# Kernel optimization log

Measured on AMD Instinct MI355X. Metric: run time of the kernel, lower is better.

Reference implementation:

```python
import jax, jax.numpy as jnp
import numpy as np

N, IN_DIM, E_DIM, H, D = 10000, 128, 32, 4, 32
NE = 640000
OUT_DIM = D  # out Linear maps H*D -> out_dim == D here (32)


def setup_inputs() -> dict:
    key = jax.random.key(0)
    ks = jax.random.split(key, 12)
    HD = H * D
    s = lambda k, sh, fan: jax.random.normal(k, sh, jnp.float32) / np.sqrt(fan)
    return {
        "x": jax.random.normal(ks[0], (N, IN_DIM), jnp.float32),
        "edge_index": jax.random.randint(ks[1], (2, NE), 0, N),
        "edge_attr": jax.random.normal(ks[2], (NE, E_DIM), jnp.float32),
        "Wq": s(ks[3], (IN_DIM, HD), IN_DIM), "bq": jnp.zeros((HD,), jnp.float32),
        "Wk": s(ks[4], (IN_DIM, HD), IN_DIM), "bk": jnp.zeros((HD,), jnp.float32),
        "Wv": s(ks[5], (IN_DIM, HD), IN_DIM), "bv": jnp.zeros((HD,), jnp.float32),
        "We": s(ks[6], (E_DIM, HD), E_DIM), "be": jnp.zeros((HD,), jnp.float32),
        "Wo": s(ks[7], (HD, OUT_DIM), HD), "bo": jnp.zeros((OUT_DIM,), jnp.float32),
    }


def reference(x, edge_index, edge_attr, Wq, bq, Wk, bk, Wv, bv, We, be, Wo, bo):
    n = x.shape[0]
    Q = (x @ Wq + bq).reshape(-1, H, D)
    K = (x @ Wk + bk).reshape(-1, H, D)
    V = (x @ Wv + bv).reshape(-1, H, D)
    Ef = (edge_attr @ We + be).reshape(-1, H, D)
    src, dst = edge_index[0], edge_index[1]
    # per-edge scores [E, H]: QK dot over src/dst gather + E self dot
    scores = (jnp.einsum('ehd,ehd->eh', Q[src], K[dst])
              + jnp.einsum('ehd,ehd->eh', Ef, Ef)) / np.sqrt(D).astype(np.float32)
    alpha = jax.nn.softmax(scores, axis=-1)  # softmax over heads (as in source)
    out_e = (alpha[..., None] * V[dst]).reshape(-1, H * D)  # [E, H*D]
    out_e = out_e @ Wo + bo  # [E, out_dim]
    # scatter-mean by source node
    sums = jax.ops.segment_sum(out_e, src, num_segments=n)
    cnt = jax.ops.segment_sum(jnp.ones((out_e.shape[0],), out_e.dtype), src, num_segments=n)
    return sums / jnp.maximum(cnt, 1.0)[:, None]
```

## Files before the change

kernel.cpp:

```cpp
#include <hip/hip_runtime.h>

#define NN      10000
#define IN_DIM  128
#define E_DIM   32
#define NH      4
#define DH      32
#define HD      128
#define NE_     640000
#define OUT_DIM 32
#define SCAN_T  1024
#define CHUNK   10
#define NTILES  (NN / 16)
#define NTASKS  (NTILES * 3)
#define QKVP_BLKS  469
#define HIST_BLKS  (NE_ / 256)
#define EE_BLKS    (NE_ / 256)

typedef __attribute__((ext_vector_type(8))) short bf16x8;
typedef __attribute__((ext_vector_type(4))) float f32x4;

static __device__ __forceinline__ unsigned short f32_to_bf16_rne(float f) {
    unsigned u = __float_as_uint(f);
    return (unsigned short)((u + 0x7fffu + ((u >> 16) & 1u)) >> 16);
}
static __device__ __forceinline__ float bf16_bits_to_f32(unsigned short h) {
    return __uint_as_float(((unsigned)h) << 16);
}

__global__ __launch_bounds__(256) void prep_kernel(
    const float* __restrict__ Wq, const float* __restrict__ Wk,
    const float* __restrict__ Wv, const float* __restrict__ Wo,
    const float* __restrict__ bv, const float* __restrict__ We,
    const int*   __restrict__ ei,
    unsigned short* __restrict__ wfh, unsigned short* __restrict__ wfl,
    unsigned short* __restrict__ wefh, unsigned short* __restrict__ wefl,
    float* __restrict__ bp,
    int* __restrict__ deg, int* __restrict__ rank)
{
    const int blk = blockIdx.x;
    const int t = threadIdx.x;

    if (blk < 24) {
        const int tid = blk * 256 + t;
        const int l = tid & 63;
        const int ts = tid >> 6;
        const int s = ts & 3, tt = ts >> 2;
        const int col = (tt & 7) * 16 + (l & 15);
        if (tt < 16) {
            const float* __restrict__ W = (tt < 8) ? Wq : Wk;
            #pragma unroll
            for (int j = 0; j < 8; ++j) {
                const int k = s * 32 + (l >> 4) * 8 + j;
                const float w = W[k * HD + col];
                const unsigned short hi = f32_to_bf16_rne(w);
                wfh[tid * 8 + j] = hi;
                wfl[tid * 8 + j] = f32_to_bf16_rne(w - bf16_bits_to_f32(hi));
            }
        } else {
            const int h = col & 3, oo = col >> 2;
            #pragma unroll
            for (int j = 0; j < 8; ++j) {
                const int k = s * 32 + (l >> 4) * 8 + j;
                float acc = 0.f;
                #pragma unroll
                for (int d2 = 0; d2 < DH; ++d2)
                    acc = fmaf(Wv[k * HD + h * DH + d2],
                               Wo[(h * DH + d2) * OUT_DIM + oo], acc);
                const unsigned short hi = f32_to_bf16_rne(acc);
                wfh[tid * 8 + j] = hi;
                wfl[tid * 8 + j] = f32_to_bf16_rne(acc - bf16_bits_to_f32(hi));
            }
        }
    } else if (blk < 26) {
        const int tid = (blk - 24) * 256 + t;
        const int l = tid & 63, tt = tid >> 6;
        #pragma unroll
        for (int j = 0; j < 8; ++j) {
            const int k = (l >> 4) * 8 + j;
            const int d = tt * 16 + (l & 15);
            const float w = We[k * HD + d];
            const unsigned short hi = f32_to_bf16_rne(w);
            wefh[tid * 8 + j] = hi;
            wefl[tid * 8 + j] = f32_to_bf16_rne(w - bf16_bits_to_f32(hi));
        }
    } else if (blk == 26) {
        if (t < HD) {
            const int h = t & 3, oo = t >> 2;
            float b = 0.f;
            #pragma unroll
            for (int d2 = 0; d2 < DH; ++d2)
                b = fmaf(bv[h * DH + d2], Wo[(h * DH + d2) * OUT_DIM + oo], b);
            bp[t] = b;
        }
    } else {
        const int e = (blk - 27) * 256 + t;
        rank[e] = atomicAdd(&deg[ei[e]], 1);
    }
}

__global__ __launch_bounds__(SCAN_T) void scan_kernel(
    const int* __restrict__ deg, int* __restrict__ off)
{
    __shared__ int wsum[16];
    const int t = threadIdx.x;
    const int lane = t & 63, w = t >> 6;
    const int base = t * CHUNK;
    int v[CHUNK];
    int sum = 0;
    #pragma unroll
    for (int i = 0; i < CHUNK; ++i) {
        const int idx = base + i;
        v[i] = (idx < NN) ? deg[idx] : 0;
        sum += v[i];
    }
    int incl = sum;
    #pragma unroll
    for (int dlt = 1; dlt < 64; dlt <<= 1) {
        const int nb = __shfl_up(incl, dlt, 64);
        if (lane >= dlt) incl += nb;
    }
    if (lane == 63) wsum[w] = incl;
    __syncthreads();
    if (w == 0) {
        const int val = (lane < 16) ? wsum[lane] : 0;
        int wi = val;
        #pragma unroll
        for (int dlt = 1; dlt < 16; dlt <<= 1) {
            const int nb = __shfl_up(wi, dlt, 64);
            if (lane >= dlt) wi += nb;
        }
        if (lane < 16) wsum[lane] = wi - val;
    }
    __syncthreads();
    int run = wsum[w] + (incl - sum);
    #pragma unroll
    for (int i = 0; i < CHUNK; ++i) {
        const int idx = base + i;
        if (idx < NN) { off[idx] = run; run += v[i]; }
    }
}

__global__ __launch_bounds__(256) void mm_kernel(
    const float* __restrict__ x,
    const unsigned short* __restrict__ wfh, const unsigned short* __restrict__ wfl,
    const float* __restrict__ bq, const float* __restrict__ bk,
    const float* __restrict__ bp,
    float* __restrict__ Q, unsigned short* __restrict__ KPTb,
    const float* __restrict__ ea,
    const unsigned short* __restrict__ wefh, const unsigned short* __restrict__ wefl,
    const float* __restrict__ be,
    const int* __restrict__ ei,
    const int* __restrict__ off, const int* __restrict__ rank,
    float4* __restrict__ pay)
{
    const int lane = threadIdx.x & 63;
    const int wave = threadIdx.x >> 6;

    if (blockIdx.x < QKVP_BLKS) {
        const int task = blockIdx.x * 4 + wave;
        if (task >= NTASKS) return;
        const int nt = task / 3, cg = task - nt * 3;
        const int node = nt * 16 + (lane & 15);
        const int kc = lane >> 4;

        bf16x8 xh0, xl0, xh1, xl1, xh2, xl2, xh3, xl3;
#define SPL(VH, VL, I, VAL) { \
    const unsigned short hh = f32_to_bf16_rne(VAL); \
    VH[I] = (short)hh; VL[I] = (short)f32_to_bf16_rne((VAL) - bf16_bits_to_f32(hh)); }
#define LOAD_X(S, VH, VL) { \
    const float* xr = x + (size_t)node * IN_DIM + (S) * 32 + kc * 8; \
    const float4 a0 = *reinterpret_cast<const float4*>(xr); \
    const float4 a1 = *reinterpret_cast<const float4*>(xr + 4); \
    SPL(VH, VL, 0, a0.x) SPL(VH, VL, 1, a0.y) SPL(VH, VL, 2, a0.z) SPL(VH, VL, 3, a0.w) \
    SPL(VH, VL, 4, a1.x) SPL(VH, VL, 5, a1.y) SPL(VH, VL, 6, a1.z) SPL(VH, VL, 7, a1.w) }
        LOAD_X(0, xh0, xl0) LOAD_X(1, xh1, xl1) LOAD_X(2, xh2, xl2) LOAD_X(3, xh3, xl3)
#undef LOAD_X
#undef SPL

        const float* __restrict__ bb = (cg == 0) ? bq : (cg == 1) ? bk : bp;

#define KSTEP(S, FB, FB2, XH, XL) { \
    const bf16x8 wh = *reinterpret_cast<const bf16x8*>((FB)  + (S) * 64 * 8); \
    const bf16x8 wl = *reinterpret_cast<const bf16x8*>((FB2) + (S) * 64 * 8); \
    acc = __builtin_amdgcn_mfma_f32_16x16x32_bf16(wh, XH, acc, 0, 0, 0); \
    acc = __builtin_amdgcn_mfma_f32_16x16x32_bf16(wh, XL, acc, 0, 0, 0); \
    acc = __builtin_amdgcn_mfma_f32_16x16x32_bf16(wl, XH, acc, 0, 0, 0); }

#define TILE(TLOC) { \
    const unsigned short* fb  = wfh + ((((cg * 8 + TLOC) * 4) * 64 + lane) << 3); \
    const unsigned short* fb2 = wfl + ((((cg * 8 + TLOC) * 4) * 64 + lane) << 3); \
    f32x4 acc = {0.f, 0.f, 0.f, 0.f}; \
    KSTEP(0, fb, fb2, xh0, xl0) KSTEP(1, fb, fb2, xh1, xl1) \
    KSTEP(2, fb, fb2, xh2, xl2) KSTEP(3, fb, fb2, xh3, xl3) \
    const float4 b4 = *reinterpret_cast<const float4*>(bb + (TLOC) * 16 + (kc << 2)); \
    const float o0 = acc[0] + b4.x, o1 = acc[1] + b4.y; \
    const float o2 = acc[2] + b4.z, o3 = acc[3] + b4.w; \
    const int j0 = (TLOC) * 16 + (kc << 2); \
    if (cg == 0) { \
        *reinterpret_cast<float4*>(Q + (size_t)node * HD + j0) = \
            make_float4(o0, o1, o2, o3); \
    } else { \
        unsigned short* dp = KPTb + (size_t)node * 256 + j0 * 2 + ((cg == 1) ? 0 : 4); \
        *reinterpret_cast<ushort4*>(dp) = make_ushort4( \
            f32_to_bf16_rne(o0), f32_to_bf16_rne(o1), \
            f32_to_bf16_rne(o2), f32_to_bf16_rne(o3)); \
    } }

        TILE(0) TILE(1) TILE(2) TILE(3) TILE(4) TILE(5) TILE(6) TILE(7)
#undef TILE
#undef KSTEP
        return;
    }

    const int base = (blockIdx.x - QKVP_BLKS) * 256 + wave * 64;

    const int src  = ei[base + lane];
    const int dstn = ei[NE_ + base + lane];
    const int pos  = off[src] + rank[base + lane];

    const int erow = lane & 15;
    const int kc = lane >> 4;
    bf16x8 ah0, ah1, ah2, ah3;
#define LOAD_A(AT, VAR) { \
    const float* ar = ea + (size_t)(base + AT * 16 + erow) * E_DIM + kc * 8; \
    const float4 a0 = *reinterpret_cast<const float4*>(ar); \
    const float4 a1 = *reinterpret_cast<const float4*>(ar + 4); \
    VAR[0] = (short)f32_to_bf16_rne(a0.x); VAR[1] = (short)f32_to_bf16_rne(a0.y); \
    VAR[2] = (short)f32_to_bf16_rne(a0.z); VAR[3] = (short)f32_to_bf16_rne(a0.w); \
    VAR[4] = (short)f32_to_bf16_rne(a1.x); VAR[5] = (short)f32_to_bf16_rne(a1.y); \
    VAR[6] = (short)f32_to_bf16_rne(a1.z); VAR[7] = (short)f32_to_bf16_rne(a1.w); }
    LOAD_A(0, ah0) LOAD_A(1, ah1) LOAD_A(2, ah2) LOAD_A(3, ah3)
#undef LOAD_A

    float p00 = 0.f, p01 = 0.f, p02 = 0.f, p03 = 0.f;
    float p10 = 0.f, p11 = 0.f, p12 = 0.f, p13 = 0.f;
    float p20 = 0.f, p21 = 0.f, p22 = 0.f, p23 = 0.f;
    float p30 = 0.f, p31 = 0.f, p32 = 0.f, p33 = 0.f;

#define AT_BODY(AT, H, WHI, WLO, BE4) { \
    f32x4 acc = {0.f, 0.f, 0.f, 0.f}; \
    acc = __builtin_amdgcn_mfma_f32_16x16x32_bf16(WLO, ah##AT, acc, 0, 0, 0); \
    acc = __builtin_amdgcn_mfma_f32_16x16x32_bf16(WHI, ah##AT, acc, 0, 0, 0); \
    const float e0 = acc[0] + BE4.x, e1 = acc[1] + BE4.y; \
    const float e2 = acc[2] + BE4.z, e3 = acc[3] + BE4.w; \
    p##AT##H += e0 * e0 + e1 * e1 + e2 * e2 + e3 * e3; }

#define TILE(T, H) { \
    const bf16x8 whi = *reinterpret_cast<const bf16x8*>(wefh + ((T * 64 + lane) << 3)); \
    const bf16x8 wlo = *reinterpret_cast<const bf16x8*>(wefl + ((T * 64 + lane) << 3)); \
    const float4 be4 = *reinterpret_cast<const float4*>(be + T * 16 + ((lane >> 4) << 2)); \
    AT_BODY(0, H, whi, wlo, be4) AT_BODY(1, H, whi, wlo, be4) \
    AT_BODY(2, H, whi, wlo, be4) AT_BODY(3, H, whi, wlo, be4) }

    TILE(0, 0) TILE(1, 0) TILE(2, 1) TILE(3, 1)
    TILE(4, 2) TILE(5, 2) TILE(6, 3) TILE(7, 3)
#undef TILE
#undef AT_BODY

#define RED(AT, H) \
    float r##AT##H = p##AT##H; \
    r##AT##H += __shfl_xor(r##AT##H, 16, 64); \
    r##AT##H += __shfl_xor(r##AT##H, 32, 64);
    RED(0, 0) RED(0, 1) RED(0, 2) RED(0, 3)
    RED(1, 0) RED(1, 1) RED(1, 2) RED(1, 3)
    RED(2, 0) RED(2, 1) RED(2, 2) RED(2, 3)
    RED(3, 0) RED(3, 1) RED(3, 2) RED(3, 3)
#undef RED

    const int at4 = lane >> 4;
#define SEL(H) ((at4 & 2) ? ((at4 & 1) ? r3##H : r2##H) : ((at4 & 1) ? r1##H : r0##H))
    const float w0 = SEL(0), w1 = SEL(1), w2 = SEL(2), w3 = SEL(3);
#undef SEL

    pay[pos] = make_float4(__int_as_float(dstn), w0 - w3, w1 - w3, w2 - w3);
}

static __device__ __forceinline__ float edge_term(
    const uint4 u, const float4 pc, const float4 q4, const int h)
{
    const float scale = 0.17677669529663687f;
    const float k0 = __uint_as_float(u.x << 16);
    const float k1 = __uint_as_float(u.x & 0xffff0000u);
    const float k2 = __uint_as_float(u.y << 16);
    const float k3 = __uint_as_float(u.y & 0xffff0000u);
    float p =           q4.x * k0;
    p = fmaf(q4.y, k1, p); p = fmaf(q4.z, k2, p); p = fmaf(q4.w, k3, p);
    p += __shfl_xor(p, 1, 64);
    p += __shfl_xor(p, 2, 64);
    p += __shfl_xor(p, 4, 64);
    const float b  = __shfl_xor(p, 8, 64);
    const float e0 = (h & 1) ? b : p;
    const float e1 = (h & 1) ? p : b;
    const float o0 = __shfl_xor(e0, 16, 64);
    const float o1 = __shfl_xor(e1, 16, 64);
    const float qk0 = (h & 2) ? o0 : e0;
    const float qk1 = (h & 2) ? o1 : e1;
    const float qk2 = (h & 2) ? e0 : o0;
    const float qk3 = (h & 2) ? e1 : o1;

    const float s0 = (qk0 + pc.y) * scale;
    const float s1 = (qk1 + pc.z) * scale;
    const float s2 = (qk2 + pc.w) * scale;
    const float s3 = qk3 * scale;
    const float mx = fmaxf(fmaxf(s0, s1), fmaxf(s2, s3));
    const float a0 = __expf(s0 - mx), a1 = __expf(s1 - mx);
    const float a2 = __expf(s2 - mx), a3 = __expf(s3 - mx);
    const float inv = 1.f / (a0 + a1 + a2 + a3);
    const float p0 = __uint_as_float(u.z << 16);
    const float p1 = __uint_as_float(u.z & 0xffff0000u);
    const float p2 = __uint_as_float(u.w << 16);
    const float p3 = __uint_as_float(u.w & 0xffff0000u);
    return fmaf(a0, p0, fmaf(a1, p1, fmaf(a2, p2, a3 * p3))) * inv;
}

__global__ __launch_bounds__(256) void fused_gather_kernel(
    const int* __restrict__ off, const int* __restrict__ deg,
    const float4* __restrict__ pay,
    const float* __restrict__ Q, const unsigned short* __restrict__ KPTb,
    const float* __restrict__ bo, float* __restrict__ out)
{
    __shared__ float red[8][OUT_DIM];
    const int n = blockIdx.x;
    const int d = deg[n];
    const int start = off[n];
    const int tid = threadIdx.x;
    const int g = tid >> 5, o = tid & 31;
    const int h = o >> 3;

    const float4 q4 = *reinterpret_cast<const float4*>(Q + (size_t)n * HD + o * 4);

    float acc = 0.f;
    float4 pc0 = make_float4(0.f, 0.f, 0.f, 0.f);
    float4 pc1 = make_float4(0.f, 0.f, 0.f, 0.f);
    if (g < d)     pc0 = pay[start + g];
    if (g + 8 < d) pc1 = pay[start + g + 8];

    for (int i = g; i < d; i += 16) {
        float4 pn0 = make_float4(0.f, 0.f, 0.f, 0.f);
        float4 pn1 = make_float4(0.f, 0.f, 0.f, 0.f);
        if (i + 16 < d) pn0 = pay[start + i + 16];
        if (i + 24 < d) pn1 = pay[start + i + 24];

        const int dst0 = __float_as_int(pc0.x);
        const int dst1 = __float_as_int(pc1.x);
        const uint4 u0 = *reinterpret_cast<const uint4*>(KPTb + (size_t)dst0 * 256 + o * 8);
        const uint4 u1 = *reinterpret_cast<const uint4*>(KPTb + (size_t)dst1 * 256 + o * 8);

        acc += edge_term(u0, pc0, q4, h);
        if (i + 8 < d)
            acc += edge_term(u1, pc1, q4, h);

        pc0 = pn0; pc1 = pn1;
    }
    red[g][o] = acc;
    __syncthreads();
    if (tid < 32) {
        const float s = red[0][o] + red[1][o] + red[2][o] + red[3][o]
                      + red[4][o] + red[5][o] + red[6][o] + red[7][o];
        out[(size_t)n * OUT_DIM + o] = (d > 0) ? (s / (float)d + bo[o]) : 0.f;
    }
}

extern "C" void kernel_launch(void* const* d_in, const int* in_sizes, int n_in,
                              void* d_out, int out_size, void* d_ws, size_t ws_size,
                              hipStream_t stream)
{
    const float* x   = (const float*)d_in[0];
    const int*   ei  = (const int*)  d_in[1];
    const float* ea  = (const float*)d_in[2];
    const float* Wq  = (const float*)d_in[3];
    const float* bq  = (const float*)d_in[4];
    const float* Wk  = (const float*)d_in[5];
    const float* bk  = (const float*)d_in[6];
    const float* Wv  = (const float*)d_in[7];
    const float* bv  = (const float*)d_in[8];
    const float* We  = (const float*)d_in[9];
    const float* be  = (const float*)d_in[10];
    const float* Wo  = (const float*)d_in[11];
    const float* bo  = (const float*)d_in[12];
    float* out = (float*)d_out;

    float*  Q    = (float*)d_ws;
    float4* pay  = (float4*)(Q + (size_t)NN * HD);
    unsigned short* KPTb = (unsigned short*)(pay + NE_);
    float*  bp   = (float*)(KPTb + (size_t)NN * 256);
    unsigned short* wefh = (unsigned short*)(bp + HD);
    unsigned short* wefl = wefh + 8 * 64 * 8;
    unsigned short* wfh  = wefl + 8 * 64 * 8;
    unsigned short* wfl  = wfh + 24 * 4 * 64 * 8;
    int* rank = (int*)(wfl + 24 * 4 * 64 * 8);
    int* deg  = rank + NE_;
    int* off  = deg + NN;

    hipMemsetAsync(deg, 0, NN * sizeof(int), stream);

    prep_kernel<<<27 + HIST_BLKS, 256, 0, stream>>>(Wq, Wk, Wv, Wo, bv, We, ei,
                                                    wfh, wfl, wefh, wefl, bp,
                                                    deg, rank);
    scan_kernel<<<1, SCAN_T, 0, stream>>>(deg, off);
    mm_kernel<<<QKVP_BLKS + EE_BLKS, 256, 0, stream>>>(x, wfh, wfl, bq, bk, bp,
                                                       Q, KPTb, ea, wefh, wefl,
                                                       be, ei, off, rank, pay);
    fused_gather_kernel<<<NN, 256, 0, stream>>>(off, deg, pay, Q, KPTb, bo, out);
}
```

Baseline: 134.0 us.

## Write edge payloads coalesced with sorted id indirection; widen gather to 16 lanes per edge

The edge kernel now writes each edge's payload (dst and score terms) coalesced, in original edge order, and scatters only a 4-byte edge id into the per-source sorted slot. The gather kernel reads the id, then the payload, which adds a level of indirection. In exchange the 16-byte scattered writes become 4-byte ones. The gather now uses 16 threads per edge, each handling 8 features and two output columns, so 16 edges are in flight per block. Biases are folded into the MFMA accumulator initialisation, and the self-dot is rewritten as an FMA chain.

Measured after the change: 127.9 us. 4.5% less time.

```diff
diff --git a/kernel.cpp b/kernel.cpp
--- a/kernel.cpp
+++ b/kernel.cpp
@@ -26,6 +26,8 @@
 static __device__ __forceinline__ float bf16_bits_to_f32(unsigned short h) {
     return __uint_as_float(((unsigned)h) << 16);
 }
+static __device__ __forceinline__ float blo(unsigned u) { return __uint_as_float(u << 16); }
+static __device__ __forceinline__ float bhi(unsigned u) { return __uint_as_float(u & 0xffff0000u); }
 
 __global__ __launch_bounds__(256) void prep_kernel(
     const float* __restrict__ Wq, const float* __restrict__ Wk,
@@ -151,7 +153,7 @@
     const float* __restrict__ be,
     const int* __restrict__ ei,
     const int* __restrict__ off, const int* __restrict__ rank,
-    float4* __restrict__ pay)
+    float4* __restrict__ eev, int* __restrict__ ids)
 {
     const int lane = threadIdx.x & 63;
     const int wave = threadIdx.x >> 6;
@@ -189,21 +191,19 @@
 #define TILE(TLOC) { \
     const unsigned short* fb  = wfh + ((((cg * 8 + TLOC) * 4) * 64 + lane) << 3); \
     const unsigned short* fb2 = wfl + ((((cg * 8 + TLOC) * 4) * 64 + lane) << 3); \
-    f32x4 acc = {0.f, 0.f, 0.f, 0.f}; \
+    const float4 b4 = *reinterpret_cast<const float4*>(bb + (TLOC) * 16 + (kc << 2)); \
+    f32x4 acc = {b4.x, b4.y, b4.z, b4.w}; \
     KSTEP(0, fb, fb2, xh0, xl0) KSTEP(1, fb, fb2, xh1, xl1) \
     KSTEP(2, fb, fb2, xh2, xl2) KSTEP(3, fb, fb2, xh3, xl3) \
-    const float4 b4 = *reinterpret_cast<const float4*>(bb + (TLOC) * 16 + (kc << 2)); \
-    const float o0 = acc[0] + b4.x, o1 = acc[1] + b4.y; \
-    const float o2 = acc[2] + b4.z, o3 = acc[3] + b4.w; \
     const int j0 = (TLOC) * 16 + (kc << 2); \
     if (cg == 0) { \
         *reinterpret_cast<float4*>(Q + (size_t)node * HD + j0) = \
-            make_float4(o0, o1, o2, o3); \
+            make_float4(acc[0], acc[1], acc[2], acc[3]); \
     } else { \
         unsigned short* dp = KPTb + (size_t)node * 256 + j0 * 2 + ((cg == 1) ? 0 : 4); \
         *reinterpret_cast<ushort4*>(dp) = make_ushort4( \
-            f32_to_bf16_rne(o0), f32_to_bf16_rne(o1), \
-            f32_to_bf16_rne(o2), f32_to_bf16_rne(o3)); \
+            f32_to_bf16_rne(acc[0]), f32_to_bf16_rne(acc[1]), \
+            f32_to_bf16_rne(acc[2]), f32_to_bf16_rne(acc[3])); \
     } }
 
         TILE(0) TILE(1) TILE(2) TILE(3) TILE(4) TILE(5) TILE(6) TILE(7)
@@ -238,12 +238,11 @@
     float p30 = 0.f, p31 = 0.f, p32 = 0.f, p33 = 0.f;
 
 #define AT_BODY(AT, H, WHI, WLO, BE4) { \
-    f32x4 acc = {0.f, 0.f, 0.f, 0.f}; \
+    f32x4 acc = {BE4.x, BE4.y, BE4.z, BE4.w}; \
     acc = __builtin_amdgcn_mfma_f32_16x16x32_bf16(WLO, ah##AT, acc, 0, 0, 0); \
     acc = __builtin_amdgcn_mfma_f32_16x16x32_bf16(WHI, ah##AT, acc, 0, 0, 0); \
-    const float e0 = acc[0] + BE4.x, e1 = acc[1] + BE4.y; \
-    const float e2 = acc[2] + BE4.z, e3 = acc[3] + BE4.w; \
-    p##AT##H += e0 * e0 + e1 * e1 + e2 * e2 + e3 * e3; }
+    p##AT##H = fmaf(acc[0], acc[0], fmaf(acc[1], acc[1], \
+               fmaf(acc[2], acc[2], fmaf(acc[3], acc[3], p##AT##H)))); }
 
 #define TILE(T, H) { \
     const bf16x8 whi = *reinterpret_cast<const bf16x8*>(wefh + ((T * 64 + lane) << 3)); \
@@ -272,92 +271,98 @@
     const float w0 = SEL(0), w1 = SEL(1), w2 = SEL(2), w3 = SEL(3);
 #undef SEL
 
-    pay[pos] = make_float4(__int_as_float(dstn), w0 - w3, w1 - w3, w2 - w3);
-}
-
-static __device__ __forceinline__ float edge_term(
-    const uint4 u, const float4 pc, const float4 q4, const int h)
-{
-    const float scale = 0.17677669529663687f;
-    const float k0 = __uint_as_float(u.x << 16);
-    const float k1 = __uint_as_float(u.x & 0xffff0000u);
-    const float k2 = __uint_as_float(u.y << 16);
-    const float k3 = __uint_as_float(u.y & 0xffff0000u);
-    float p =           q4.x * k0;
-    p = fmaf(q4.y, k1, p); p = fmaf(q4.z, k2, p); p = fmaf(q4.w, k3, p);
-    p += __shfl_xor(p, 1, 64);
-    p += __shfl_xor(p, 2, 64);
-    p += __shfl_xor(p, 4, 64);
-    const float b  = __shfl_xor(p, 8, 64);
-    const float e0 = (h & 1) ? b : p;
-    const float e1 = (h & 1) ? p : b;
-    const float o0 = __shfl_xor(e0, 16, 64);
-    const float o1 = __shfl_xor(e1, 16, 64);
-    const float qk0 = (h & 2) ? o0 : e0;
-    const float qk1 = (h & 2) ? o1 : e1;
-    const float qk2 = (h & 2) ? e0 : o0;
-    const float qk3 = (h & 2) ? e1 : o1;
-
-    const float s0 = (qk0 + pc.y) * scale;
-    const float s1 = (qk1 + pc.z) * scale;
-    const float s2 = (qk2 + pc.w) * scale;
-    const float s3 = qk3 * scale;
-    const float mx = fmaxf(fmaxf(s0, s1), fmaxf(s2, s3));
-    const float a0 = __expf(s0 - mx), a1 = __expf(s1 - mx);
-    const float a2 = __expf(s2 - mx), a3 = __expf(s3 - mx);
-    const float inv = 1.f / (a0 + a1 + a2 + a3);
-    const float p0 = __uint_as_float(u.z << 16);
-    const float p1 = __uint_as_float(u.z & 0xffff0000u);
-    const float p2 = __uint_as_float(u.w << 16);
-    const float p3 = __uint_as_float(u.w & 0xffff0000u);
-    return fmaf(a0, p0, fmaf(a1, p1, fmaf(a2, p2, a3 * p3))) * inv;
+    eev[base + lane] = make_float4(__int_as_float(dstn), w0 - w3, w1 - w3, w2 - w3);
+    ids[pos] = base + lane;
 }
 
 __global__ __launch_bounds__(256) void fused_gather_kernel(
     const int* __restrict__ off, const int* __restrict__ deg,
-    const float4* __restrict__ pay,
+    const int* __restrict__ ids, const float4* __restrict__ eev,
     const float* __restrict__ Q, const unsigned short* __restrict__ KPTb,
     const float* __restrict__ bo, float* __restrict__ out)
 {
-    __shared__ float red[8][OUT_DIM];
+    __shared__ float red[16][OUT_DIM];
     const int n = blockIdx.x;
     const int d = deg[n];
     const int start = off[n];
     const int tid = threadIdx.x;
-    const int g = tid >> 5, o = tid & 31;
-    const int h = o >> 3;
-
-    const float4 q4 = *reinterpret_cast<const float4*>(Q + (size_t)n * HD + o * 4);
-
-    float acc = 0.f;
-    float4 pc0 = make_float4(0.f, 0.f, 0.f, 0.f);
-    float4 pc1 = make_float4(0.f, 0.f, 0.f, 0.f);
-    if (g < d)     pc0 = pay[start + g];
-    if (g + 8 < d) pc1 = pay[start + g + 8];
+    const int g = tid >> 4;
+    const int o16 = tid & 15;
+    const int h = o16 >> 2;
+    const float scale = 0.17677669529663687f;
+
+    const float* __restrict__ qrow = Q + (size_t)n * HD + o16 * 8;
+    const float4 qa = *reinterpret_cast<const float4*>(qrow);
+    const float4 qb = *reinterpret_cast<const float4*>(qrow + 4);
+
+    float acc0 = 0.f, acc1 = 0.f;
+
+    float4 pc = make_float4(0.f, 0.f, 0.f, 0.f);
+    int idn = 0;
+    if (g < d)      pc  = eev[ids[start + g]];
+    if (g + 16 < d) idn = ids[start + g + 16];
 
     for (int i = g; i < d; i += 16) {
-        float4 pn0 = make_float4(0.f, 0.f, 0.f, 0.f);
-        float4 pn1 = make_float4(0.f, 0.f, 0.f, 0.f);
-        if (i + 16 < d) pn0 = pay[start + i + 16];
-        if (i + 24 < d) pn1 = pay[start + i + 24];
-
-        const int dst0 = __float_as_int(pc0.x);
-        const int dst1 = __float_as_int(pc1.x);
-        const uint4 u0 = *reinterpret_cast<const uint4*>(KPTb + (size_t)dst0 * 256 + o * 8);
-        const uint4 u1 = *reinterpret_cast<const uint4*>(KPTb + (size_t)dst1 * 256 + o * 8);
-
-        acc += edge_term(u0, pc0, q4, h);
-        if (i + 8 < d)
-            acc += edge_term(u1, pc1, q4, h);
-
-        pc0 = pn0; pc1 = pn1;
-    }
-    red[g][o] = acc;
+        int idn2 = 0;
+        if (i + 32 < d) idn2 = ids[start + i + 32];
+        float4 pn = make_float4(0.f, 0.f, 0.f, 0.f);
+        if (i + 16 < d) pn = eev[idn];
+
+        const int dst = __float_as_int(pc.x);
+        const unsigned short* __restrict__ kp = KPTb + (size_t)dst * 256 + o16 * 16;
+        const uint4 u0 = *reinterpret_cast<const uint4*>(kp);
+        const uint4 u1 = *reinterpret_cast<const uint4*>(kp + 8);
+
+        float p =           qa.x * blo(u0.x);
+        p = fmaf(qa.y, bhi(u0.x), p);
+        p = fmaf(qa.z, blo(u0.y), p);
+        p = fmaf(qa.w, bhi(u0.y), p);
+        p = fmaf(qb.x, blo(u1.x), p);
+        p = fmaf(qb.y, bhi(u1.x), p);
+        p = fmaf(qb.z, blo(u1.y), p);
+        p = fmaf(qb.w, bhi(u1.y), p);
+        p += __shfl_xor(p, 1, 64);
+        p += __shfl_xor(p, 2, 64);
+        const float b  = __shfl_xor(p, 4, 64);
+        const float e0 = (h & 1) ? b : p;
+        const float e1 = (h & 1) ? p : b;
+        const float o0 = __shfl_xor(e0, 8, 64);
+        const float o1 = __shfl_xor(e1, 8, 64);
+        const float qk0 = (h & 2) ? o0 : e0;
+        const float qk1 = (h & 2) ? o1 : e1;
+        const float qk2 = (h & 2) ? e0 : o0;
+        const float qk3 = (h & 2) ? e1 : o1;
+
+        const float s0 = (qk0 + pc.y) * scale;
+        const float s1 = (qk1 + pc.z) * scale;
+        const float s2 = (qk2 + pc.w) * scale;
+        const float s3 = qk3 * scale;
+        const float mx = fmaxf(fmaxf(s0, s1), fmaxf(s2, s3));
+        const float a0 = __expf(s0 - mx), a1 = __expf(s1 - mx);
+        const float a2 = __expf(s2 - mx), a3 = __expf(s3 - mx);
+        const float inv = 1.f / (a0 + a1 + a2 + a3);
+
+        float c0 =          a0 * blo(u0.z);
+        c0 = fmaf(a1, bhi(u0.z), c0);
+        c0 = fmaf(a2, blo(u0.w), c0);
+        c0 = fmaf(a3, bhi(u0.w), c0);
+        float c1 =          a0 * blo(u1.z);
+        c1 = fmaf(a1, bhi(u1.z), c1);
+        c1 = fmaf(a2, blo(u1.w), c1);
+        c1 = fmaf(a3, bhi(u1.w), c1);
+        acc0 = fmaf(c0, inv, acc0);
+        acc1 = fmaf(c1, inv, acc1);
+
+        pc = pn; idn = idn2;
+    }
+    red[g][o16 * 2]     = acc0;
+    red[g][o16 * 2 + 1] = acc1;
     __syncthreads();
     if (tid < 32) {
-        const float s = red[0][o] + red[1][o] + red[2][o] + red[3][o]
-                      + red[4][o] + red[5][o] + red[6][o] + red[7][o];
-        out[(size_t)n * OUT_DIM + o] = (d > 0) ? (s / (float)d + bo[o]) : 0.f;
+        float s = 0.f;
+        #pragma unroll
+        for (int gg = 0; gg < 16; ++gg) s += red[gg][tid];
+        out[(size_t)n * OUT_DIM + tid] = (d > 0) ? (s / (float)d + bo[tid]) : 0.f;
     }
 }
 
@@ -381,15 +386,16 @@
     float* out = (float*)d_out;
 
     float*  Q    = (float*)d_ws;
-    float4* pay  = (float4*)(Q + (size_t)NN * HD);
-    unsigned short* KPTb = (unsigned short*)(pay + NE_);
+    float4* eev  = (float4*)(Q + (size_t)NN * HD);
+    unsigned short* KPTb = (unsigned short*)(eev + NE_);
     float*  bp   = (float*)(KPTb + (size_t)NN * 256);
     unsigned short* wefh = (unsigned short*)(bp + HD);
     unsigned short* wefl = wefh + 8 * 64 * 8;
     unsigned short* wfh  = wefl + 8 * 64 * 8;
     unsigned short* wfl  = wfh + 24 * 4 * 64 * 8;
     int* rank = (int*)(wfl + 24 * 4 * 64 * 8);
-    int* deg  = rank + NE_;
+    int* ids  = rank + NE_;
+    int* deg  = ids + NE_;
     int* off  = deg + NN;
 
     hipMemsetAsync(deg, 0, NN * sizeof(int), stream);
@@ -400,6 +406,6 @@
     scan_kernel<<<1, SCAN_T, 0, stream>>>(deg, off);
     mm_kernel<<<QKVP_BLKS + EE_BLKS, 256, 0, stream>>>(x, wfh, wfl, bq, bk, bp,
                                                        Q, KPTb, ea, wefh, wefl,
-                                                       be, ei, off, rank, pay);
-    fused_gather_kernel<<<NN, 256, 0, stream>>>(off, deg, pay, Q, KPTb, bo, out);
-}
+                                                       be, ei, off, rank, eev, ids);
+    fused_gather_kernel<<<NN, 256, 0, stream>>>(off, deg, ids, eev, Q, KPTb, bo, out);
+}
```
